# Kernel tuning notes

Hardware: AMD Instinct MI355X
Metric: run time of the kernel (lower is better)

## Reference

```python
import jax, jax.numpy as jnp
import numpy as np

N = 100_000   # nodes
E = 1_600_000 # edges (avg degree 16)
D = 64        # in_dim == hidden_dim


def setup_inputs() -> dict:
    key = jax.random.key(0)
    ks = jax.random.split(key, 9)
    scale = 1.0 / np.sqrt(D)
    x = jax.random.normal(ks[0], (N, D), jnp.float32)
    edge_index = jax.random.randint(ks[1], (2, E), 0, N, dtype=jnp.int32)
    W0 = jax.random.normal(ks[2], (D, D), jnp.float32) * scale
    b0 = jnp.zeros((D,), jnp.float32)
    W1 = jax.random.normal(ks[3], (D, D), jnp.float32) * scale
    b1 = jnp.zeros((D,), jnp.float32)
    W2 = jax.random.normal(ks[4], (D, D), jnp.float32) * scale
    b2 = jnp.zeros((D,), jnp.float32)
    return {"x": x, "edge_index": edge_index, "W0": W0, "b0": b0,
            "W1": W1, "b1": b1, "W2": W2, "b2": b2}


def _gcn_layer(h, W, b, src, dst, norm):
    # h: [N, D]; src/dst: [E+N] (self-loops included); norm: [E+N]
    h = h @ W                                  # dense transform [N, D]
    msg = h[src] * norm[:, None]               # gather + scale  [E+N, D]
    out = jax.ops.segment_sum(msg, dst, num_segments=N)  # scatter-add [N, D]
    return out + b


def reference(x, edge_index, W0, b0, W1, b1, W2, b2):
    loops = jnp.arange(N, dtype=edge_index.dtype)
    src = jnp.concatenate([edge_index[0], loops])  # [E+N]
    dst = jnp.concatenate([edge_index[1], loops])  # [E+N]
    # symmetric GCN normalization with self-loops (PyG gcn_norm)
    deg = jax.ops.segment_sum(jnp.ones_like(dst, dtype=x.dtype), dst, num_segments=N)
    d_inv = jnp.where(deg > 0, jax.lax.rsqrt(deg), 0.0)
    norm = d_inv[src] * d_inv[dst]                 # [E+N]
    for W, b in ((W0, b0), (W1, b1), (W2, b2)):
        x = jax.nn.relu(_gcn_layer(x, W, b, src, dst, norm))
    return x
```

## Files before the change

kernel.cpp:

```cpp
#include <hip/hip_runtime.h>
#include <hip/hip_fp16.h>


#define THREADS 256
#define BSH     9
#define BNODES  512
#define BCAP    9216
#define BPAD    16
#define CHUNK   4096

#if defined(__has_builtin)
#if __has_builtin(__builtin_amdgcn_fdot2) && __has_builtin(__builtin_amdgcn_perm)
#define USE_DOT2 1
#endif
#endif

typedef __attribute__((ext_vector_type(2))) _Float16 h2v;
typedef __attribute__((ext_vector_type(8))) _Float16 f16x8;
typedef __attribute__((ext_vector_type(4))) float    f32x4;

__global__ __launch_bounds__(THREADS)
void bin_kernel(const int* __restrict__ src, const int* __restrict__ dst,
                int* __restrict__ bcur, int* __restrict__ sbuf, int E) {
    __shared__ int cntb[THREADS];
    __shared__ int lstart[THREADS];
    __shared__ int gbase[THREADS];
    __shared__ int lcur[THREADS];
    __shared__ int tmp[THREADS];
    __shared__ int stagep[CHUNK];
    __shared__ unsigned char stageb[CHUNK];
    int tid = threadIdx.x;
    int e0  = blockIdx.x * CHUNK;
    int cnt = min(CHUNK, E - e0);
    int dreg[16];
#pragma unroll
    for (int j = 0; j < 16; ++j) {
        int i = tid + j * THREADS;
        dreg[j] = (i < cnt) ? dst[e0 + i] : -1;
    }
    cntb[tid] = 0;
    __syncthreads();
#pragma unroll
    for (int j = 0; j < 16; ++j)
        if (dreg[j] >= 0) atomicAdd(&cntb[dreg[j] >> BSH], 1);
    __syncthreads();
    int v = cntb[tid];
    tmp[tid] = v;
    __syncthreads();
    for (int off = 1; off < THREADS; off <<= 1) {
        int t = (tid >= off) ? tmp[tid - off] : 0;
        __syncthreads();
        tmp[tid] += t;
        __syncthreads();
    }
    lstart[tid] = tmp[tid] - v;
    lcur[tid]   = 0;
    if (v > 0) gbase[tid] = atomicAdd(&bcur[tid * BPAD], v);
    __syncthreads();
#pragma unroll
    for (int j = 0; j < 16; ++j) {
        int i = tid + j * THREADS;
        if (i < cnt) {
            int s = src[e0 + i];
            int d = dreg[j];
            int b = d >> BSH;
            int pos = atomicAdd(&lcur[b], 1);
            int idx = lstart[b] + pos;
            stagep[idx] = (s << BSH) | (d & (BNODES - 1));
            stageb[idx] = (unsigned char)b;
        }
    }
    __syncthreads();
    for (int i = tid; i < cnt; i += THREADS) {
        int b = stageb[i];
        sbuf[(size_t)b * BCAP + gbase[b] + (i - lstart[b])] = stagep[i];
    }
}

__global__ __launch_bounds__(THREADS)
void bscan_kernel(const int* __restrict__ bcur, int* __restrict__ bbase,
                  int NB, int* __restrict__ rowptr, int N, int E) {
    __shared__ int tmp[THREADS];
    int tid = threadIdx.x;
    int c = (tid < NB) ? min(bcur[tid * BPAD], BCAP) : 0;
    tmp[tid] = c;
    __syncthreads();
    for (int off = 1; off < THREADS; off <<= 1) {
        int t = (tid >= off) ? tmp[tid - off] : 0;
        __syncthreads();
        tmp[tid] += t;
        __syncthreads();
    }
    if (tid < NB) bbase[tid] = tmp[tid] - c;
    if (tid == 0) rowptr[N] = E;
}

__global__ __launch_bounds__(THREADS)
void finalize_kernel(const int* __restrict__ sbuf, const int* __restrict__ bcur,
                     const int* __restrict__ bbase, int* __restrict__ rowptr,
                     float* __restrict__ dinv, int* __restrict__ csrc, int N) {
    __shared__ int lcnt[BNODES];
    __shared__ int lexcl[BNODES];
    __shared__ int lcur[BNODES];
    __shared__ int tmp[THREADS];
    int b   = blockIdx.x;
    int tid = threadIdx.x;
    int cnt = min(bcur[b * BPAD], BCAP);
    int gb  = bbase[b];
    const int* sb = sbuf + (size_t)b * BCAP;
    for (int i = tid; i < BNODES; i += THREADS) { lcnt[i] = 0; lcur[i] = 0; }
    __syncthreads();
    for (int e = tid; e < cnt; e += THREADS)
        atomicAdd(&lcnt[sb[e] & (BNODES - 1)], 1);
    __syncthreads();
    int a0 = lcnt[2 * tid], a1 = lcnt[2 * tid + 1];
    int s  = a0 + a1;
    tmp[tid] = s;
    __syncthreads();
    for (int off = 1; off < THREADS; off <<= 1) {
        int t = (tid >= off) ? tmp[tid - off] : 0;
        __syncthreads();
        tmp[tid] += t;
        __syncthreads();
    }
    int ex = tmp[tid] - s;
    lexcl[2 * tid]     = ex;
    lexcl[2 * tid + 1] = ex + a0;
    int node = (b << BSH) + 2 * tid;
    if (node < N) {
        rowptr[node] = gb + ex;
        dinv[node]   = rsqrtf((float)(a0 + 1));
    }
    if (node + 1 < N) {
        rowptr[node + 1] = gb + ex + a0;
        dinv[node + 1]   = rsqrtf((float)(a1 + 1));
    }
    __syncthreads();
    for (int e = tid; e < cnt; e += THREADS) {
        int vv  = sb[e];
        int d   = vv & (BNODES - 1);
        int pos = atomicAdd(&lcur[d], 1);
        csrc[gb + lexcl[d] + pos] = vv >> BSH;
    }
}

__global__ __launch_bounds__(THREADS)
void gemm64_kernel(const float* __restrict__ X, __half* __restrict__ H,
                   const float* __restrict__ W, const float* __restrict__ dinv,
                   int n) {
    int lane = threadIdx.x & 63;
    int qk   = lane >> 4;
    int l16  = lane & 15;
    f16x8 bf[4][2];
#pragma unroll
    for (int t = 0; t < 4; ++t)
#pragma unroll
        for (int h = 0; h < 2; ++h) {
            const float* wp = W + (size_t)(32 * h + qk * 8) * 64 + 16 * t + l16;
#pragma unroll
            for (int j = 0; j < 8; ++j)
                bf[t][h][j] = (_Float16)wp[j * 64];
        }
    int wave  = (blockIdx.x * blockDim.x + threadIdx.x) >> 6;
    int nw    = (gridDim.x * blockDim.x) >> 6;
    int ntile = (n + 15) >> 4;
    for (int tile = wave; tile < ntile; tile += nw) {
        int rbase = tile << 4;
        int arow  = rbase + l16;
        if (arow >= n) arow = n - 1;
        const float4* xp = (const float4*)(X + (size_t)arow * 64 + qk * 8);
        float4 a0 = xp[0], a1 = xp[1];
        float4 a2 = xp[8], a3 = xp[9];
        f16x8 A0, A1;
        A0[0] = (_Float16)a0.x; A0[1] = (_Float16)a0.y;
        A0[2] = (_Float16)a0.z; A0[3] = (_Float16)a0.w;
        A0[4] = (_Float16)a1.x; A0[5] = (_Float16)a1.y;
        A0[6] = (_Float16)a1.z; A0[7] = (_Float16)a1.w;
        A1[0] = (_Float16)a2.x; A1[1] = (_Float16)a2.y;
        A1[2] = (_Float16)a2.z; A1[3] = (_Float16)a2.w;
        A1[4] = (_Float16)a3.x; A1[5] = (_Float16)a3.y;
        A1[6] = (_Float16)a3.z; A1[7] = (_Float16)a3.w;
        f32x4 acc[4];
#pragma unroll
        for (int t = 0; t < 4; ++t) {
            acc[t] = (f32x4){0.f, 0.f, 0.f, 0.f};
            acc[t] = __builtin_amdgcn_mfma_f32_16x16x32_f16(A0, bf[t][0], acc[t], 0, 0, 0);
            acc[t] = __builtin_amdgcn_mfma_f32_16x16x32_f16(A1, bf[t][1], acc[t], 0, 0, 0);
        }
#pragma unroll
        for (int r = 0; r < 4; ++r) {
            int row = rbase + qk * 4 + r;
            if (row < n) {
                float dv = dinv[row];
                __half* hp = H + (size_t)row * 64 + l16;
#pragma unroll
                for (int t = 0; t < 4; ++t)
                    hp[16 * t] = __float2half(acc[t][r] * dv);
            }
        }
    }
}

__device__ __forceinline__ void pairdot(const int4& hA, const int4& hB,
                                        bool vA, bool vB, float* accf) {
#ifdef USE_DOT2
    unsigned mb = (vA ? 0x3C00u : 0u) | (vB ? 0x3C000000u : 0u);
    h2v m2 = __builtin_bit_cast(h2v, mb);
    const unsigned* pa = (const unsigned*)&hA;
    const unsigned* pb = (const unsigned*)&hB;
#pragma unroll
    for (int j = 0; j < 4; ++j) {
        unsigned p0 = __builtin_amdgcn_perm(pb[j], pa[j], 0x05040100);
        unsigned p1 = __builtin_amdgcn_perm(pb[j], pa[j], 0x07060302);
        accf[2 * j]     = __builtin_amdgcn_fdot2(
            __builtin_bit_cast(h2v, p0), m2, accf[2 * j], false);
        accf[2 * j + 1] = __builtin_amdgcn_fdot2(
            __builtin_bit_cast(h2v, p1), m2, accf[2 * j + 1], false);
    }
#else
    float mA = vA ? 1.f : 0.f, mB = vB ? 1.f : 0.f;
    const __half2* ha = (const __half2*)&hA;
    const __half2* hb = (const __half2*)&hB;
#pragma unroll
    for (int j = 0; j < 4; ++j) {
        float2 fa = __half22float2(ha[j]);
        float2 fb = __half22float2(hb[j]);
        accf[2 * j]     = fmaf(fa.x, mA, accf[2 * j]);
        accf[2 * j]     = fmaf(fb.x, mB, accf[2 * j]);
        accf[2 * j + 1] = fmaf(fa.y, mA, accf[2 * j + 1]);
        accf[2 * j + 1] = fmaf(fb.y, mB, accf[2 * j + 1]);
    }
#endif
}

__global__ __launch_bounds__(THREADS)
void agg_kernel(const __half* __restrict__ H, float* __restrict__ Y,
                const int* __restrict__ rowptr, const int* __restrict__ csrc,
                const float* __restrict__ dinv, const float* __restrict__ bias,
                int n) {
    int lane = threadIdx.x & 63;
    int half = lane >> 5;
    int hl   = lane & 31;
    int grp  = hl >> 3;
    int sub  = lane & 7;
    int fl   = sub * 8;
    const int4* H4 = (const int4*)H;
    int wave = (blockIdx.x * blockDim.x + threadIdx.x) >> 6;
    int nw   = (gridDim.x * blockDim.x) >> 6;
    int np   = (n + 1) >> 1;
    float4 bv0 = *(const float4*)(bias + fl);
    float4 bv1 = *(const float4*)(bias + fl + 4);
    int wp = wave;
    if (wp >= np) return;
    int node = min(2 * wp + half, n - 1);
    int k0 = rowptr[node], k1 = rowptr[node + 1];
    while (true) {
        int wpn = wp + nw;
        int noden = 0, k0n = 0, k1n = 0;
        bool more = wpn < np;
        if (more) {
            noden = min(2 * wpn + half, n - 1);
            k0n = rowptr[noden];
            k1n = rowptr[noden + 1];
        }
        float accf[8] = {0.f, 0.f, 0.f, 0.f, 0.f, 0.f, 0.f, 0.f};
        {
            int4 hv = H4[(size_t)node * 8 + sub];
            if (grp == 0) {
                const __half2* hh = (const __half2*)&hv;
#pragma unroll
                for (int j = 0; j < 4; ++j) {
                    float2 f = __half22float2(hh[j]);
                    accf[2 * j]     += f.x;
                    accf[2 * j + 1] += f.y;
                }
            }
        }
        for (int basek = k0; basek < k1; basek += 16) {
            int  kk0 = basek + grp;
            int  kk1 = kk0 + 4, kk2 = kk0 + 8, kk3 = kk0 + 12;
            bool v0 = kk0 < k1, v1 = kk1 < k1, v2 = kk2 < k1, v3 = kk3 < k1;
            int  s0 = v0 ? csrc[kk0] : 0;
            int  s1 = v1 ? csrc[kk1] : 0;
            int  s2 = v2 ? csrc[kk2] : 0;
            int  s3 = v3 ? csrc[kk3] : 0;
            int4 h0 = H4[(size_t)s0 * 8 + sub];
            int4 h1 = H4[(size_t)s1 * 8 + sub];
            int4 h2 = H4[(size_t)s2 * 8 + sub];
            int4 h3 = H4[(size_t)s3 * 8 + sub];
            pairdot(h0, h1, v0, v1, accf);
            pairdot(h2, h3, v2, v3, accf);
        }
#pragma unroll
        for (int j = 0; j < 8; ++j) {
            float a = accf[j];
            a += __shfl_xor(a, 8);
            a += __shfl_xor(a, 16);
            accf[j] = a;
        }
        if (grp == 0 && 2 * wp + half < n) {
            float di = dinv[node];
            float4 o0, o1;
            o0.x = fmaxf(fmaf(accf[0], di, bv0.x), 0.f);
            o0.y = fmaxf(fmaf(accf[1], di, bv0.y), 0.f);
            o0.z = fmaxf(fmaf(accf[2], di, bv0.z), 0.f);
            o0.w = fmaxf(fmaf(accf[3], di, bv0.w), 0.f);
            o1.x = fmaxf(fmaf(accf[4], di, bv1.x), 0.f);
            o1.y = fmaxf(fmaf(accf[5], di, bv1.y), 0.f);
            o1.z = fmaxf(fmaf(accf[6], di, bv1.z), 0.f);
            o1.w = fmaxf(fmaf(accf[7], di, bv1.w), 0.f);
            *(float4*)(Y + (size_t)node * 64 + fl)     = o0;
            *(float4*)(Y + (size_t)node * 64 + fl + 4) = o1;
        }
        if (!more) break;
        wp = wpn; node = noden; k0 = k0n; k1 = k1n;
    }
}

extern "C" void kernel_launch(void* const* d_in, const int* in_sizes, int n_in,
                              void* d_out, int out_size, void* d_ws, size_t ws_size,
                              hipStream_t stream) {
    const float* x  = (const float*)d_in[0];
    const int*   ei = (const int*)d_in[1];
    const float* W0 = (const float*)d_in[2];
    const float* b0 = (const float*)d_in[3];
    const float* W1 = (const float*)d_in[4];
    const float* b1 = (const float*)d_in[5];
    const float* W2 = (const float*)d_in[6];
    const float* b2 = (const float*)d_in[7];

    const int N = in_sizes[0] / 64;
    const int E = in_sizes[1] / 2;
    const int* src = ei;
    const int* dst = ei + E;
    const int NB = (N + BNODES - 1) >> BSH;

    char*  ws  = (char*)d_ws;
    size_t off = 0;
    auto alloc = [&](size_t bytes) -> void* {
        void* p = ws + off;
        off += (bytes + 255) & ~(size_t)255;
        return p;
    };
    int*    rowptr = (int*)   alloc((size_t)(N + 1) * 4);
    float*  dinv   = (float*) alloc((size_t)N * 4);
    int*    csrc   = (int*)   alloc((size_t)E * 4);
    int*    bcur   = (int*)   alloc((size_t)NB * BPAD * 4);
    int*    bbase  = (int*)   alloc((size_t)NB * 4);
    float*  actA   = (float*) alloc((size_t)N * 64 * 4);
    __half* hbuf   = (__half*)alloc((size_t)N * 64 * 2);
    int*    sbuf   = (int*)actA;
    float*  outb   = (float*)d_out;

    hipMemsetAsync(bcur, 0, (size_t)NB * BPAD * 4, stream);

    const int ngrid = 2048;
    const int ggrid = 1024;
    const int bgrid = (E + CHUNK - 1) / CHUNK;

    bin_kernel     <<<bgrid, THREADS, 0, stream>>>(src, dst, bcur, sbuf, E);
    bscan_kernel   <<<1,     THREADS, 0, stream>>>(bcur, bbase, NB, rowptr, N, E);
    finalize_kernel<<<NB,    THREADS, 0, stream>>>(sbuf, bcur, bbase, rowptr,
                                                   dinv, csrc, N);

    gemm64_kernel<<<ggrid, THREADS, 0, stream>>>(x, hbuf, W0, dinv, N);
    agg_kernel   <<<ngrid, THREADS, 0, stream>>>(hbuf, actA, rowptr, csrc, dinv, b0, N);
    gemm64_kernel<<<ggrid, THREADS, 0, stream>>>(actA, hbuf, W1, dinv, N);
    agg_kernel   <<<ngrid, THREADS, 0, stream>>>(hbuf, outb, rowptr, csrc, dinv, b1, N);
    gemm64_kernel<<<ggrid, THREADS, 0, stream>>>(outb, hbuf, W2, dinv, N);
    agg_kernel   <<<ngrid, THREADS, 0, stream>>>(hbuf, outb, rowptr, csrc, dinv, b2, N);
}
```

Baseline: 185.2 us.

## Store intermediate activations in fp16 and software-pipeline first neighbor gather in aggregation

Intermediate layer activations are written by the aggregation kernel as fp16 and read directly as fp16 MFMA operands by the next GEMM, which halves activation traffic and drops the conversion step. The aggregation kernel also prefetches the next node's first block of neighbor indices and issues its H gathers at the top of the loop, to hide gather latency. The memset is replaced with a small zero kernel, and sbuf gets its own workspace buffer instead of aliasing the activation buffer. Rounding activations to fp16 adds some precision loss, and the extra prefetched registers add register pressure.

```diff
diff --git a/kernel.cpp b/kernel.cpp
--- a/kernel.cpp
+++ b/kernel.cpp
@@ -18,6 +18,12 @@
 typedef __attribute__((ext_vector_type(2))) _Float16 h2v;
 typedef __attribute__((ext_vector_type(8))) _Float16 f16x8;
 typedef __attribute__((ext_vector_type(4))) float    f32x4;
+
+__global__ __launch_bounds__(THREADS)
+void zero_kernel(int* __restrict__ p, int n) {
+    int i = blockIdx.x * blockDim.x + threadIdx.x;
+    if (i < n) p[i] = 0;
+}
 
 __global__ __launch_bounds__(THREADS)
 void bin_kernel(const int* __restrict__ src, const int* __restrict__ dst,
@@ -144,8 +150,9 @@
     }
 }
 
-__global__ __launch_bounds__(THREADS)
-void gemm64_kernel(const float* __restrict__ X, __half* __restrict__ H,
+template <typename IT>
+__global__ __launch_bounds__(THREADS)
+void gemm64_kernel(const IT* __restrict__ X, __half* __restrict__ H,
                    const float* __restrict__ W, const float* __restrict__ dinv,
                    int n) {
     int lane = threadIdx.x & 63;
@@ -168,18 +175,24 @@
         int rbase = tile << 4;
         int arow  = rbase + l16;
         if (arow >= n) arow = n - 1;
-        const float4* xp = (const float4*)(X + (size_t)arow * 64 + qk * 8);
-        float4 a0 = xp[0], a1 = xp[1];
-        float4 a2 = xp[8], a3 = xp[9];
         f16x8 A0, A1;
-        A0[0] = (_Float16)a0.x; A0[1] = (_Float16)a0.y;
-        A0[2] = (_Float16)a0.z; A0[3] = (_Float16)a0.w;
-        A0[4] = (_Float16)a1.x; A0[5] = (_Float16)a1.y;
-        A0[6] = (_Float16)a1.z; A0[7] = (_Float16)a1.w;
-        A1[0] = (_Float16)a2.x; A1[1] = (_Float16)a2.y;
-        A1[2] = (_Float16)a2.z; A1[3] = (_Float16)a2.w;
-        A1[4] = (_Float16)a3.x; A1[5] = (_Float16)a3.y;
-        A1[6] = (_Float16)a3.z; A1[7] = (_Float16)a3.w;
+        if constexpr (sizeof(IT) == 4) {
+            const float4* xp = (const float4*)((const float*)X + (size_t)arow * 64 + qk * 8);
+            float4 a0 = xp[0], a1 = xp[1];
+            float4 a2 = xp[8], a3 = xp[9];
+            A0[0] = (_Float16)a0.x; A0[1] = (_Float16)a0.y;
+            A0[2] = (_Float16)a0.z; A0[3] = (_Float16)a0.w;
+            A0[4] = (_Float16)a1.x; A0[5] = (_Float16)a1.y;
+            A0[6] = (_Float16)a1.z; A0[7] = (_Float16)a1.w;
+            A1[0] = (_Float16)a2.x; A1[1] = (_Float16)a2.y;
+            A1[2] = (_Float16)a2.z; A1[3] = (_Float16)a2.w;
+            A1[4] = (_Float16)a3.x; A1[5] = (_Float16)a3.y;
+            A1[6] = (_Float16)a3.z; A1[7] = (_Float16)a3.w;
+        } else {
+            const int4* xp = (const int4*)((const __half*)X + (size_t)arow * 64 + qk * 8);
+            A0 = __builtin_bit_cast(f16x8, xp[0]);
+            A1 = __builtin_bit_cast(f16x8, xp[4]);
+        }
         f32x4 acc[4];
 #pragma unroll
         for (int t = 0; t < 4; ++t) {
@@ -233,8 +246,9 @@
 #endif
 }
 
-__global__ __launch_bounds__(THREADS)
-void agg_kernel(const __half* __restrict__ H, float* __restrict__ Y,
+template <typename OT>
+__global__ __launch_bounds__(THREADS)
+void agg_kernel(const __half* __restrict__ H, OT* __restrict__ Y,
                 const int* __restrict__ rowptr, const int* __restrict__ csrc,
                 const float* __restrict__ dinv, const float* __restrict__ bias,
                 int n) {
@@ -254,42 +268,59 @@
     if (wp >= np) return;
     int node = min(2 * wp + half, n - 1);
     int k0 = rowptr[node], k1 = rowptr[node + 1];
+    int  kk = k0 + grp;
+    bool v0 = kk < k1, v1 = kk + 4 < k1, v2 = kk + 8 < k1, v3 = kk + 12 < k1;
+    int  s0 = v0 ? csrc[kk] : 0;
+    int  s1 = v1 ? csrc[kk + 4] : 0;
+    int  s2 = v2 ? csrc[kk + 8] : 0;
+    int  s3 = v3 ? csrc[kk + 12] : 0;
     while (true) {
+        int4 h0 = H4[(size_t)s0 * 8 + sub];
+        int4 h1 = H4[(size_t)s1 * 8 + sub];
+        int4 h2 = H4[(size_t)s2 * 8 + sub];
+        int4 h3 = H4[(size_t)s3 * 8 + sub];
+        int4 hv = H4[(size_t)node * 8 + sub];
         int wpn = wp + nw;
-        int noden = 0, k0n = 0, k1n = 0;
         bool more = wpn < np;
+        int noden = 0, k0n = 0, k1n = 0, s0n = 0, s1n = 0, s2n = 0, s3n = 0;
+        bool v0n = false, v1n = false, v2n = false, v3n = false;
         if (more) {
             noden = min(2 * wpn + half, n - 1);
             k0n = rowptr[noden];
             k1n = rowptr[noden + 1];
+            int kkn = k0n + grp;
+            v0n = kkn < k1n; v1n = kkn + 4 < k1n;
+            v2n = kkn + 8 < k1n; v3n = kkn + 12 < k1n;
+            s0n = v0n ? csrc[kkn] : 0;
+            s1n = v1n ? csrc[kkn + 4] : 0;
+            s2n = v2n ? csrc[kkn + 8] : 0;
+            s3n = v3n ? csrc[kkn + 12] : 0;
         }
         float accf[8] = {0.f, 0.f, 0.f, 0.f, 0.f, 0.f, 0.f, 0.f};
-        {
-            int4 hv = H4[(size_t)node * 8 + sub];
-            if (grp == 0) {
-                const __half2* hh = (const __half2*)&hv;
-#pragma unroll
-                for (int j = 0; j < 4; ++j) {
-                    float2 f = __half22float2(hh[j]);
-                    accf[2 * j]     += f.x;
-                    accf[2 * j + 1] += f.y;
-                }
+        if (grp == 0) {
+            const __half2* hh = (const __half2*)&hv;
+#pragma unroll
+            for (int j = 0; j < 4; ++j) {
+                float2 f = __half22float2(hh[j]);
+                accf[2 * j]     += f.x;
+                accf[2 * j + 1] += f.y;
             }
         }
-        for (int basek = k0; basek < k1; basek += 16) {
-            int  kk0 = basek + grp;
-            int  kk1 = kk0 + 4, kk2 = kk0 + 8, kk3 = kk0 + 12;
-            bool v0 = kk0 < k1, v1 = kk1 < k1, v2 = kk2 < k1, v3 = kk3 < k1;
-            int  s0 = v0 ? csrc[kk0] : 0;
-            int  s1 = v1 ? csrc[kk1] : 0;
-            int  s2 = v2 ? csrc[kk2] : 0;
-            int  s3 = v3 ? csrc[kk3] : 0;
-            int4 h0 = H4[(size_t)s0 * 8 + sub];
-            int4 h1 = H4[(size_t)s1 * 8 + sub];
-            int4 h2 = H4[(size_t)s2 * 8 + sub];
-            int4 h3 = H4[(size_t)s3 * 8 + sub];
-            pairdot(h0, h1, v0, v1, accf);
-            pairdot(h2, h3, v2, v3, accf);
+        pairdot(h0, h1, v0, v1, accf);
+        pairdot(h2, h3, v2, v3, accf);
+        for (int basek = k0 + 16; basek < k1; basek += 16) {
+            int  ka = basek + grp, kb = ka + 4, kc = ka + 8, kd = ka + 12;
+            bool va = ka < k1, vb = kb < k1, vc = kc < k1, vd = kd < k1;
+            int  sa = va ? csrc[ka] : 0;
+            int  sb = vb ? csrc[kb] : 0;
+            int  sc = vc ? csrc[kc] : 0;
+            int  sd = vd ? csrc[kd] : 0;
+            int4 ha = H4[(size_t)sa * 8 + sub];
+            int4 hb = H4[(size_t)sb * 8 + sub];
+            int4 hc = H4[(size_t)sc * 8 + sub];
+            int4 hd = H4[(size_t)sd * 8 + sub];
+            pairdot(ha, hb, va, vb, accf);
+            pairdot(hc, hd, vc, vd, accf);
         }
 #pragma unroll
         for (int j = 0; j < 8; ++j) {
@@ -300,20 +331,33 @@
         }
         if (grp == 0 && 2 * wp + half < n) {
             float di = dinv[node];
-            float4 o0, o1;
-            o0.x = fmaxf(fmaf(accf[0], di, bv0.x), 0.f);
-            o0.y = fmaxf(fmaf(accf[1], di, bv0.y), 0.f);
-            o0.z = fmaxf(fmaf(accf[2], di, bv0.z), 0.f);
-            o0.w = fmaxf(fmaf(accf[3], di, bv0.w), 0.f);
-            o1.x = fmaxf(fmaf(accf[4], di, bv1.x), 0.f);
-            o1.y = fmaxf(fmaf(accf[5], di, bv1.y), 0.f);
-            o1.z = fmaxf(fmaf(accf[6], di, bv1.z), 0.f);
-            o1.w = fmaxf(fmaf(accf[7], di, bv1.w), 0.f);
-            *(float4*)(Y + (size_t)node * 64 + fl)     = o0;
-            *(float4*)(Y + (size_t)node * 64 + fl + 4) = o1;
+            float o[8];
+            o[0] = fmaxf(fmaf(accf[0], di, bv0.x), 0.f);
+            o[1] = fmaxf(fmaf(accf[1], di, bv0.y), 0.f);
+            o[2] = fmaxf(fmaf(accf[2], di, bv0.z), 0.f);
+            o[3] = fmaxf(fmaf(accf[3], di, bv0.w), 0.f);
+            o[4] = fmaxf(fmaf(accf[4], di, bv1.x), 0.f);
+            o[5] = fmaxf(fmaf(accf[5], di, bv1.y), 0.f);
+            o[6] = fmaxf(fmaf(accf[6], di, bv1.z), 0.f);
+            o[7] = fmaxf(fmaf(accf[7], di, bv1.w), 0.f);
+            if constexpr (sizeof(OT) == 2) {
+                __half2 hh[4];
+#pragma unroll
+                for (int j = 0; j < 4; ++j)
+                    hh[j] = __floats2half2_rn(o[2 * j], o[2 * j + 1]);
+                *(int4*)((__half*)Y + (size_t)node * 64 + fl) =
+                    *(const int4*)hh;
+            } else {
+                float4 o0 = make_float4(o[0], o[1], o[2], o[3]);
+                float4 o1 = make_float4(o[4], o[5], o[6], o[7]);
+                *(float4*)((float*)Y + (size_t)node * 64 + fl)     = o0;
+                *(float4*)((float*)Y + (size_t)node * 64 + fl + 4) = o1;
+            }
         }
         if (!more) break;
         wp = wpn; node = noden; k0 = k0n; k1 = k1n;
+        v0 = v0n; v1 = v1n; v2 = v2n; v3 = v3n;
+        s0 = s0n; s1 = s1n; s2 = s2n; s3 = s3n;
     }
 }
 
@@ -347,26 +391,26 @@
     int*    csrc   = (int*)   alloc((size_t)E * 4);
     int*    bcur   = (int*)   alloc((size_t)NB * BPAD * 4);
     int*    bbase  = (int*)   alloc((size_t)NB * 4);
-    float*  actA   = (float*) alloc((size_t)N * 64 * 4);
+    int*    sbuf   = (int*)   alloc((size_t)NB * BCAP * 4);
     __half* hbuf   = (__half*)alloc((size_t)N * 64 * 2);
-    int*    sbuf   = (int*)actA;
+    __half* act16  = (__half*)alloc((size_t)N * 64 * 2);
     float*  outb   = (float*)d_out;
-
-    hipMemsetAsync(bcur, 0, (size_t)NB * BPAD * 4, stream);
 
     const int ngrid = 2048;
     const int ggrid = 1024;
     const int bgrid = (E + CHUNK - 1) / CHUNK;
-
+    const int zn    = NB * BPAD;
+
+    zero_kernel    <<<(zn + THREADS - 1) / THREADS, THREADS, 0, stream>>>(bcur, zn);
     bin_kernel     <<<bgrid, THREADS, 0, stream>>>(src, dst, bcur, sbuf, E);
     bscan_kernel   <<<1,     THREADS, 0, stream>>>(bcur, bbase, NB, rowptr, N, E);
     finalize_kernel<<<NB,    THREADS, 0, stream>>>(sbuf, bcur, bbase, rowptr,
                                                    dinv, csrc, N);
 
-    gemm64_kernel<<<ggrid, THREADS, 0, stream>>>(x, hbuf, W0, dinv, N);
-    agg_kernel   <<<ngrid, THREADS, 0, stream>>>(hbuf, actA, rowptr, csrc, dinv, b0, N);
-    gemm64_kernel<<<ggrid, THREADS, 0, stream>>>(actA, hbuf, W1, dinv, N);
-    agg_kernel   <<<ngrid, THREADS, 0, stream>>>(hbuf, outb, rowptr, csrc, dinv, b1, N);
-    gemm64_kernel<<<ggrid, THREADS, 0, stream>>>(outb, hbuf, W2, dinv, N);
-    agg_kernel   <<<ngrid, THREADS, 0, stream>>>(hbuf, outb, rowptr, csrc, dinv, b2, N);
-}
+    gemm64_kernel<float> <<<ggrid, THREADS, 0, stream>>>(x, hbuf, W0, dinv, N);
+    agg_kernel<__half>   <<<ngrid, THREADS, 0, stream>>>(hbuf, act16, rowptr, csrc, dinv, b0, N);
+    gemm64_kernel<__half><<<ggrid, THREADS, 0, stream>>>(act16, hbuf, W1, dinv, N);
+    agg_kernel<__half>   <<<ngrid, THREADS, 0, stream>>>(hbuf, act16, rowptr, csrc, dinv, b1, N);
+    gemm64_kernel<__half><<<ggrid, THREADS, 0, stream>>>(act16, hbuf, W2, dinv, N);
+    agg_kernel<float>    <<<ngrid, THREADS, 0, stream>>>(hbuf, outb, rowptr, csrc, dinv, b2, N);
+}
```

Measured after the change: 203.3 us. +9.7%, slower.
